# Optimization experiments

Hardware: AMD Instinct MI355X
Metric: run time of the kernel (lower is better)

Reference implementation:

```python
import jax, jax.numpy as jnp
import numpy as np

N_NODES, N_EDGES, B, K = 10000, 100000, 8192, 10
MEM = EMB = TE = EF = 172
HID = 80
MSG = 2 * MEM + TE + EF  # 688


def setup_inputs() -> dict:
    key = jax.random.key(0)
    ks = jax.random.split(key, 24)
    f = jax.random.normal
    inp = {
        'timestamps': jax.random.uniform(ks[0], (B,)) * 100.0,
        'edge_features': f(ks[1], (N_EDGES, EF)),
        'temporal_node_features': f(ks[2], (N_NODES, MEM)),
        'node_mem': 0.1 * f(ks[3], (N_NODES, MEM)),
        'last_updated': jax.random.uniform(ks[4], (N_NODES,)) * 50.0,
        'nbr_edge_times': jax.random.uniform(ks[5], (B, K)) * 100.0,
        # TimeEncode params (fixed init from source)
        'time_w': jnp.asarray(1.0 / 10 ** np.linspace(0, 9, TE), jnp.float32),
        'time_b': jnp.zeros((TE,), jnp.float32),
        # RNNCell params
        'rnn_Wih': 0.05 * f(ks[6], (MEM, MSG)),
        'rnn_Whh': 0.05 * f(ks[7], (MEM, MEM)),
        'rnn_bih': jnp.zeros((MEM,)),
        'rnn_bhh': jnp.zeros((MEM,)),
        # layer linears (n_layers=1)
        'lin1_w': 0.05 * f(ks[8], (EMB, EMB + TE + EF)),
        'lin1_b': jnp.zeros((EMB,)),
        'lin2_w': 0.05 * f(ks[9], (EMB, MEM + TE + EMB)),
        'lin2_b': jnp.zeros((EMB,)),
        # MLP head
        'mlp_w1': 0.05 * f(ks[10], (HID, EMB)),
        'mlp_b1': jnp.zeros((HID,)),
        'mlp_w2': 0.05 * f(ks[11], (10, HID)),
        'mlp_b2': jnp.zeros((10,)),
        'mlp_w3': 0.05 * f(ks[12], (1, 10)),
        'mlp_b3': jnp.zeros((1,)),
        'sources': jax.random.randint(ks[13], (B,), 0, N_NODES),
        'destinations': jax.random.randint(ks[14], (B,), 0, N_NODES),
        'edge_idxs': jax.random.randint(ks[15], (B,), 0, N_EDGES),
        'neighbors': jax.random.randint(ks[16], (B, K), 0, N_NODES),
        'nbr_edge_idxs': jax.random.randint(ks[17], (B, K), 0, N_EDGES),
    }
    return inp


def _time_enc(dt, w, b):
    # cos(Linear(1->D)(t)) from TimeEncode
    return jnp.cos(dt[..., None] * w + b)


def reference(timestamps, edge_features, temporal_node_features, node_mem,
              last_updated, nbr_edge_times, time_w, time_b,
              rnn_Wih, rnn_Whh, rnn_bih, rnn_bhh,
              lin1_w, lin1_b, lin2_w, lin2_b,
              mlp_w1, mlp_b1, mlp_w2, mlp_b2, mlp_w3, mlp_b3,
              sources, destinations, edge_idxs, neighbors, nbr_edge_idxs):
    # ---- get_message: gather memories + edge features + time-delta encoding
    ef = edge_features[edge_idxs]                         # [B, EF]
    src_mem = node_mem[sources]                           # [B, MEM]
    dst_mem = node_mem[destinations]                      # [B, MEM]
    dt = timestamps - last_updated[sources]               # [B]
    msg = jnp.concatenate([src_mem, dst_mem, ef, _time_enc(dt, time_w, time_b)], axis=1)  # [B, MSG]

    # ---- message aggregation: keep LAST message per unique source node
    n = node_mem.shape[0]
    b = sources.shape[0]
    last_idx = jnp.full((n,), -1, jnp.int32).at[sources].max(jnp.arange(b, dtype=jnp.int32))
    upd = last_idx >= 0                                   # [N] nodes receiving a message
    gi = jnp.clip(last_idx, 0)
    node_msg = msg[gi]                                    # [N, MSG]

    # ---- RNNCell memory update (masked to updated nodes)
    h_new = jnp.tanh(node_msg @ rnn_Wih.T + rnn_bih + node_mem @ rnn_Whh.T + rnn_bhh)
    mem = jnp.where(upd[:, None], h_new, node_mem)        # [N, MEM]

    # ---- compute_embedding, n_layers = 1 (layer-0 feats = mem + temporal feats)
    src_feat = mem[sources] + temporal_node_features[sources]      # [B, MEM]
    nbr_feat = mem[neighbors] + temporal_node_features[neighbors]  # [B, K, MEM]
    edge_t_enc = _time_enc(timestamps[:, None] - nbr_edge_times, time_w, time_b)  # [B, K, TE]
    nbr_ef = edge_features[nbr_edge_idxs]                           # [B, K, EF]
    nf = jnp.concatenate([nbr_feat, edge_t_enc, nbr_ef], axis=2)    # [B, K, MEM+TE+EF]
    h1 = jnp.einsum('bkf,ef->bke', nf, lin1_w) + lin1_b             # linear_1
    nbr_sum = jax.nn.relu(jnp.sum(h1, axis=1))                      # sum-aggregate, [B, EMB]
    src_t_enc = _time_enc(jnp.zeros_like(timestamps), time_w, time_b)  # cos(b), [B, TE]
    emb = jnp.concatenate([nbr_sum, src_feat, src_t_enc], axis=1) @ lin2_w.T + lin2_b  # [B, EMB]

    # ---- MLP head (dropout disabled / eval mode) + sigmoid
    h = jax.nn.relu(emb @ mlp_w1.T + mlp_b1)
    h = jax.nn.relu(h @ mlp_w2.T + mlp_b2)
    return jax.nn.sigmoid((h @ mlp_w3.T + mlp_b3)[:, 0])  # [B]
```

## Files before the change

### kernel.cpp

```cpp
#include <hip/hip_runtime.h>
#include <math.h>

#define N_NODES 10000
#define BB 8192
#define KK 10
#define D 172
#define HIDD 80

typedef _Float16 f16;
typedef f16 f16x8 __attribute__((ext_vector_type(8)));
typedef f16 f16x4 __attribute__((ext_vector_type(4)));
typedef float f32x4 __attribute__((ext_vector_type(4)));


__global__ void scatter_last(const int* __restrict__ sources, int* __restrict__ last_idx) {
    int b = blockIdx.x * blockDim.x + threadIdx.x;
    if (b < BB) atomicMax(&last_idx[sources[b]], b);
}

__global__ void compact_nodes(const int* __restrict__ last_idx, int* __restrict__ nid,
                              int* __restrict__ li_arr, int* __restrict__ cnt) {
    int n = blockIdx.x * blockDim.x + threadIdx.x;
    if (n < N_NODES) {
        int li = last_idx[n];
        if (li >= 0) { int p = atomicAdd(cnt, 1); nid[p] = n; li_arr[p] = li; }
    }
}

__global__ __launch_bounds__(256) void conv_weights(
    const float* __restrict__ Wih, const float* __restrict__ Whh,
    const float* __restrict__ lin1_w, const float* __restrict__ lin2_w,
    const float* __restrict__ w1,
    const float* __restrict__ bih, const float* __restrict__ bhh,
    const float* __restrict__ lin2_b, const float* __restrict__ tb,
    const float* __restrict__ node_mem, const float* __restrict__ tnf,
    f16* __restrict__ Wc, f16* __restrict__ W1, f16* __restrict__ W2,
    f16* __restrict__ Wm1, float* __restrict__ bcomb, float* __restrict__ embc,
    f16* __restrict__ FEAT)
{
    const int which = blockIdx.y;
    const int idx = blockIdx.x * 256 + threadIdx.x;
    if (which == 0) {
        if (idx >= 192 * 704) return;
        int n = idx / 704, k = idx % 704, seg = k / 176, kk = k % 176;
        float v = 0.f;
        if (n < D && kk < D) {
            v = Wih[n * 688 + seg * D + kk];
            if (seg == 0) v += Whh[n * D + kk];
        }
        Wc[idx] = (f16)v;
    } else if (which == 1) {
        if (idx >= 192 * 544) return;
        int n = idx / 544, k = idx % 544, seg = k / 176, kk = k % 176;
        float v = 0.f;
        if (n < D && seg < 3 && kk < D) v = lin1_w[n * 516 + seg * D + kk];
        W1[idx] = (f16)v;
    } else if (which == 2) {
        if (idx >= 192 * 352) return;
        int n = idx / 352, k = idx % 352, seg = k / 176, kk = k % 176;
        float v = 0.f;
        if (n < D && kk < D) v = lin2_w[n * 516 + seg * D + kk];
        W2[idx] = (f16)v;
    } else if (which == 3) {
        if (idx >= 80 * 192) return;
        int n = idx / 192, k = idx % 192;
        Wm1[idx] = (f16)((k < D) ? w1[n * D + k] : 0.f);
    } else if (which == 4) {
        if (idx < D) {
            bcomb[idx] = bih[idx] + bhh[idx];
            float acc = lin2_b[idx];
            for (int j = 0; j < D; ++j) acc += lin2_w[idx * 516 + 344 + j] * __cosf(tb[j]);
            embc[idx] = acc;
        }
    } else {
        if (idx >= N_NODES * 22) return;
        int n = idx / 22, k0 = (idx % 22) * 8;
        f16x8 o;
        #pragma unroll
        for (int j = 0; j < 8; ++j) {
            int kk = k0 + j;
            float v = (kk < D) ? node_mem[(size_t)n * D + kk] + tnf[(size_t)n * D + kk] : 0.f;
            o[j] = (f16)v;
        }
        *(f16x8*)(FEAT + (size_t)n * 176 + k0) = o;
    }
}

#define LDA_R 712

__global__ __launch_bounds__(768) void gemm_rnn_fused(
    const f16* __restrict__ Wc, const float* __restrict__ bcomb,
    const int* __restrict__ nid, const int* __restrict__ li_arr, const int* __restrict__ cnt,
    const int* __restrict__ destinations, const int* __restrict__ edge_idxs,
    const float* __restrict__ timestamps, const float* __restrict__ last_updated,
    const float* __restrict__ node_mem, const float* __restrict__ edge_features,
    const float* __restrict__ tw, const float* __restrict__ tb,
    const float* __restrict__ tnf, f16* __restrict__ FEAT)
{
    const int c = *cnt;
    const int R0 = blockIdx.x * 32;
    if (R0 >= c) return;
    __shared__ f16 As[32 * LDA_R];
    __shared__ int s_n[32], s_dst[32], s_ei[32];
    __shared__ float s_dt[32];
    const int t = threadIdx.x;
    if (t < 32) {
        int i = R0 + t; if (i > c - 1) i = c - 1;
        int n = nid[i], li = li_arr[i];
        s_n[t] = n; s_dst[t] = destinations[li]; s_ei[t] = edge_idxs[li];
        s_dt[t] = timestamps[li] - last_updated[n];
    }
    __syncthreads();
    for (int idx = t; idx < 32 * 88; idx += 768) {
        int row = idx / 88, sub = idx - row * 88;
        int seg = sub / 22, cpos = sub - seg * 22, k0 = cpos * 8;
        f16x8 o;
        if (seg < 3) {
            int n = (seg == 0) ? s_n[row] : (seg == 1) ? s_dst[row] : s_ei[row];
            const float* src = ((seg < 2) ? node_mem : edge_features) + (size_t)n * D + k0;
            float4 lo = *(const float4*)src;
            float4 hi = (cpos < 21) ? *(const float4*)(src + 4) : make_float4(0.f, 0.f, 0.f, 0.f);
            o[0] = (f16)lo.x; o[1] = (f16)lo.y; o[2] = (f16)lo.z; o[3] = (f16)lo.w;
            o[4] = (f16)hi.x; o[5] = (f16)hi.y; o[6] = (f16)hi.z; o[7] = (f16)hi.w;
        } else {
            float dt = s_dt[row];
            #pragma unroll
            for (int j = 0; j < 8; ++j) {
                int kk = k0 + j;
                o[j] = (f16)((kk < D) ? __cosf(dt * tw[kk] + tb[kk]) : 0.f);
            }
        }
        *(f16x8*)(As + row * LDA_R + seg * 176 + k0) = o;
    }
    __syncthreads();
    const int w = t >> 6, l = t & 63;
    const int lane16 = l & 15, koff = (l >> 4) * 8;
    const int C0 = w * 16;
    const f16* Al0 = As + lane16 * LDA_R + koff;
    const f16* Al1 = As + (16 + lane16) * LDA_R + koff;
    const f16* Bp  = Wc + (size_t)(C0 + lane16) * 704 + koff;
    f32x4 acc0 = {}, acc1 = {};
    #pragma unroll 2
    for (int s = 0; s < 22; ++s) {
        f16x8 a0 = *(const f16x8*)(Al0 + s * 32);
        f16x8 a1 = *(const f16x8*)(Al1 + s * 32);
        f16x8 b  = *(const f16x8*)(Bp + s * 32);
        acc0 = __builtin_amdgcn_mfma_f32_16x16x32_f16(a0, b, acc0, 0, 0, 0);
        acc1 = __builtin_amdgcn_mfma_f32_16x16x32_f16(a1, b, acc1, 0, 0, 0);
    }
    const int col = C0 + lane16;
    const int rloc = (l >> 4) * 4;
    const float bc = (col < D) ? bcomb[col] : 0.f;
    if (col < D) {
        #pragma unroll
        for (int rh = 0; rh < 2; ++rh) {
            const f32x4& A = rh ? acc1 : acc0;
            #pragma unroll
            for (int reg = 0; reg < 4; ++reg) {
                int rl = rh * 16 + rloc + reg;
                int r = R0 + rl;
                if (r >= c) continue;
                int n = s_n[rl];
                FEAT[(size_t)n * 176 + col] = (f16)(tanhf(A[reg] + bc) + tnf[(size_t)n * D + col]);
            }
        }
    }
}

#define LDA_1 552

__global__ __launch_bounds__(768) void gemm_lin1_fused(
    const f16* __restrict__ W1, const float* __restrict__ lin1_b,
    const f16* __restrict__ FEAT, const float* __restrict__ edge_features,
    const float* __restrict__ timestamps, const float* __restrict__ nbr_edge_times,
    const int* __restrict__ neighbors, const int* __restrict__ nbr_edge_idxs,
    const int* __restrict__ sources,
    const float* __restrict__ tw, const float* __restrict__ tb,
    f16* __restrict__ CAT2)
{
    __shared__ f16 As[32 * LDA_1];
    __shared__ int s_nbr[320], s_nei[320], s_src[32];
    __shared__ float s_net[320], s_ts[32];
    const int t = threadIdx.x;
    const int R0 = blockIdx.x * 32;
    if (t < 320) {
        s_nbr[t] = neighbors[R0 * KK + t];
        s_nei[t] = nbr_edge_idxs[R0 * KK + t];
        s_net[t] = nbr_edge_times[R0 * KK + t];
    } else if (t < 352) {
        s_ts[t - 320] = timestamps[R0 + t - 320];
    } else if (t < 384) {
        s_src[t - 352] = sources[R0 + t - 352];
    }
    __syncthreads();
    for (int idx = t; idx < 32 * 90 + 32 * 22; idx += 768) {
        if (idx < 32 * 90) {
            int row = idx / 90, c = idx - row * 90;
            if (c < 22) {
                int k0 = c * 8;
                f16x8 v[KK];
                #pragma unroll
                for (int k = 0; k < KK; ++k)
                    v[k] = *(const f16x8*)(FEAT + (size_t)s_nbr[row * KK + k] * 176 + k0);
                float a[8] = {};
                #pragma unroll
                for (int k = 0; k < KK; ++k) {
                    #pragma unroll
                    for (int j = 0; j < 8; ++j) a[j] += (float)v[k][j];
                }
                f16x8 o;
                #pragma unroll
                for (int j = 0; j < 8; ++j) o[j] = (f16)a[j];
                *(f16x8*)(As + row * LDA_1 + k0) = o;
            } else if (c < 44) {
                int k0 = (c - 22) * 8;
                float ts = s_ts[row];
                f16x8 o;
                #pragma unroll
                for (int j = 0; j < 8; ++j) {
                    int kk = k0 + j;
                    float a = 0.f;
                    if (kk < D) {
                        float w = tw[kk], bb = tb[kk];
                        #pragma unroll
                        for (int k = 0; k < KK; ++k) a += __cosf((ts - s_net[row * KK + k]) * w + bb);
                    }
                    o[j] = (f16)a;
                }
                *(f16x8*)(As + row * LDA_1 + 176 + k0) = o;
            } else if (c < 88) {
                int cc = c - 44;
                f16x4 o;
                if (cc == 43) {
                    o[0] = o[1] = o[2] = o[3] = (f16)0.f;
                } else {
                    float4 e[KK];
                    #pragma unroll
                    for (int k = 0; k < KK; ++k)
                        e[k] = *(const float4*)(edge_features + (size_t)s_nei[row * KK + k] * D + cc * 4);
                    float a0 = 0.f, a1 = 0.f, a2 = 0.f, a3 = 0.f;
                    #pragma unroll
                    for (int k = 0; k < KK; ++k) { a0 += e[k].x; a1 += e[k].y; a2 += e[k].z; a3 += e[k].w; }
                    o[0] = (f16)a0; o[1] = (f16)a1; o[2] = (f16)a2; o[3] = (f16)a3;
                }
                *(f16x4*)(As + row * LDA_1 + 352 + cc * 4) = o;
            } else {
                f16x8 z = {};
                *(f16x8*)(As + row * LDA_1 + 528 + (c - 88) * 8) = z;
            }
        } else {
            int j = idx - 32 * 90;
            int row = j / 22, cc = j - row * 22;
            *(f16x8*)(CAT2 + (size_t)(R0 + row) * 352 + 176 + cc * 8) =
                *(const f16x8*)(FEAT + (size_t)s_src[row] * 176 + cc * 8);
        }
    }
    __syncthreads();
    const int w = t >> 6, l = t & 63;
    const int lane16 = l & 15, koff = (l >> 4) * 8;
    const int C0 = w * 16;
    const f16* Al0 = As + lane16 * LDA_1 + koff;
    const f16* Al1 = As + (16 + lane16) * LDA_1 + koff;
    const f16* Bp  = W1 + (size_t)(C0 + lane16) * 544 + koff;
    f32x4 acc0 = {}, acc1 = {};
    #pragma unroll 2
    for (int s = 0; s < 17; ++s) {
        f16x8 a0 = *(const f16x8*)(Al0 + s * 32);
        f16x8 a1 = *(const f16x8*)(Al1 + s * 32);
        f16x8 b  = *(const f16x8*)(Bp + s * 32);
        acc0 = __builtin_amdgcn_mfma_f32_16x16x32_f16(a0, b, acc0, 0, 0, 0);
        acc1 = __builtin_amdgcn_mfma_f32_16x16x32_f16(a1, b, acc1, 0, 0, 0);
    }
    const int col = C0 + lane16;
    const int rloc = (l >> 4) * 4;
    const float bb = (col < D) ? 10.0f * lin1_b[col] : 0.f;
    #pragma unroll
    for (int rh = 0; rh < 2; ++rh) {
        const f32x4& A = rh ? acc1 : acc0;
        #pragma unroll
        for (int reg = 0; reg < 4; ++reg) {
            int r = R0 + rh * 16 + rloc + reg;
            CAT2[(size_t)r * 352 + col] = (col < D) ? (f16)fmaxf(A[reg] + bb, 0.f) : (f16)0.f;
        }
    }
}

#define LDE 200

__global__ __launch_bounds__(768) void gemm_lin2_mlp(
    const f16* __restrict__ CAT2, const f16* __restrict__ W2, const float* __restrict__ embc,
    const f16* __restrict__ Wm1, const float* __restrict__ b1,
    const float* __restrict__ w2, const float* __restrict__ b2,
    const float* __restrict__ w3, const float* __restrict__ b3, float* __restrict__ out)
{
    __shared__ f16 Emb[32 * LDE];
    __shared__ float sH[32][84];
    __shared__ float s_w2[10 * HIDD];
    __shared__ float s_b2[10], s_w3[10], s_b3;
    const int t = threadIdx.x;
    const int R0 = blockIdx.x * 32;
    for (int i = t; i < 10 * HIDD; i += 768) s_w2[i] = w2[i];
    if (t < 10) { s_b2[t] = b2[t]; s_w3[t] = w3[t]; }
    if (t == 10) s_b3 = b3[0];
    const int w = t >> 6, l = t & 63;
    const int lane16 = l & 15, koff = (l >> 4) * 8;
    const int rloc = (l >> 4) * 4;
    {
        const int C0 = w * 16;
        const f16* Ap0 = CAT2 + (size_t)(R0 + lane16) * 352 + koff;
        const f16* Ap1 = CAT2 + (size_t)(R0 + 16 + lane16) * 352 + koff;
        const f16* Bp  = W2 + (size_t)(C0 + lane16) * 352 + koff;
        f32x4 acc0 = {}, acc1 = {};
        #pragma unroll 2
        for (int s = 0; s < 11; ++s) {
            f16x8 a0 = *(const f16x8*)(Ap0 + s * 32);
            f16x8 a1 = *(const f16x8*)(Ap1 + s * 32);
            f16x8 b  = *(const f16x8*)(Bp + s * 32);
            acc0 = __builtin_amdgcn_mfma_f32_16x16x32_f16(a0, b, acc0, 0, 0, 0);
            acc1 = __builtin_amdgcn_mfma_f32_16x16x32_f16(a1, b, acc1, 0, 0, 0);
        }
        const int col = C0 + lane16;
        const float ec = (col < D) ? embc[col] : 0.f;
        #pragma unroll
        for (int rh = 0; rh < 2; ++rh) {
            const f32x4& A = rh ? acc1 : acc0;
            #pragma unroll
            for (int reg = 0; reg < 4; ++reg) {
                int r = rh * 16 + rloc + reg;
                Emb[r * LDE + col] = (col < D) ? (f16)(A[reg] + ec) : (f16)0.f;
            }
        }
    }
    __syncthreads();
    if (w < 10) {
        const int C0 = (w >> 1) * 16;
        const int rh = w & 1;
        const f16* Bp = Wm1 + (size_t)(C0 + lane16) * 192 + koff;
        const f16* Al = Emb + (rh * 16 + lane16) * LDE + koff;
        f32x4 acc = {};
        #pragma unroll
        for (int s = 0; s < 6; ++s) {
            f16x8 a = *(const f16x8*)(Al + s * 32);
            f16x8 b = *(const f16x8*)(Bp + s * 32);
            acc = __builtin_amdgcn_mfma_f32_16x16x32_f16(a, b, acc, 0, 0, 0);
        }
        const int col = C0 + lane16;
        #pragma unroll
        for (int reg = 0; reg < 4; ++reg)
            sH[rh * 16 + rloc + reg][col] = fmaxf(acc[reg] + b1[col], 0.f);
    }
    __syncthreads();
    if (t < 32) {
        float h2[10];
        #pragma unroll
        for (int j = 0; j < 10; ++j) h2[j] = s_b2[j];
        for (int f = 0; f < HIDD; ++f) {
            float hv = sH[t][f];
            #pragma unroll
            for (int j = 0; j < 10; ++j) h2[j] = fmaf(hv, s_w2[j * HIDD + f], h2[j]);
        }
        float logit = s_b3;
        #pragma unroll
        for (int j = 0; j < 10; ++j) logit += fmaxf(h2[j], 0.f) * s_w3[j];
        out[R0 + t] = 1.f / (1.f + expf(-logit));
    }
}


extern "C" void kernel_launch(void* const* d_in, const int* in_sizes, int n_in,
                              void* d_out, int out_size, void* d_ws, size_t ws_size,
                              hipStream_t stream) {
    const float* timestamps     = (const float*)d_in[0];
    const float* edge_features  = (const float*)d_in[1];
    const float* tnf            = (const float*)d_in[2];
    const float* node_mem       = (const float*)d_in[3];
    const float* last_updated   = (const float*)d_in[4];
    const float* nbr_edge_times = (const float*)d_in[5];
    const float* time_w         = (const float*)d_in[6];
    const float* time_b         = (const float*)d_in[7];
    const float* Wih            = (const float*)d_in[8];
    const float* Whh            = (const float*)d_in[9];
    const float* bih            = (const float*)d_in[10];
    const float* bhh            = (const float*)d_in[11];
    const float* lin1_w         = (const float*)d_in[12];
    const float* lin1_b         = (const float*)d_in[13];
    const float* lin2_w         = (const float*)d_in[14];
    const float* lin2_b         = (const float*)d_in[15];
    const float* w1             = (const float*)d_in[16];
    const float* b1             = (const float*)d_in[17];
    const float* w2             = (const float*)d_in[18];
    const float* b2             = (const float*)d_in[19];
    const float* w3             = (const float*)d_in[20];
    const float* b3             = (const float*)d_in[21];
    const int* sources          = (const int*)d_in[22];
    const int* destinations     = (const int*)d_in[23];
    const int* edge_idxs        = (const int*)d_in[24];
    const int* neighbors        = (const int*)d_in[25];
    const int* nbr_edge_idxs    = (const int*)d_in[26];
    float* out = (float*)d_out;

    char* p = (char*)d_ws;
    auto bump = [&p](size_t bytes) { char* r = p; p += (bytes + 255) & ~(size_t)255; return r; };
    int* last_idx = (int*)bump(N_NODES * 4);
    int* nid      = (int*)bump(N_NODES * 4);
    int* li_arr   = (int*)bump(N_NODES * 4);
    int* cnt      = (int*)bump(256);
    f16* Wc16     = (f16*)bump((size_t)192 * 704 * 2);
    f16* W1_16    = (f16*)bump((size_t)192 * 544 * 2);
    f16* W2_16    = (f16*)bump((size_t)192 * 352 * 2);
    f16* Wm1_16   = (f16*)bump((size_t)80 * 192 * 2);
    float* bcomb  = (float*)bump(D * 4);
    float* embc   = (float*)bump(D * 4);
    f16* FEAT16   = (f16*)bump((size_t)N_NODES * 176 * 2);
    f16* CAT2_16  = (f16*)bump((size_t)BB * 352 * 2);

    hipMemsetAsync(last_idx, 0xFF, (size_t)N_NODES * 4, stream);
    hipMemsetAsync(cnt, 0, 4, stream);
    hipLaunchKernelGGL(scatter_last, dim3(BB / 256), dim3(256), 0, stream, sources, last_idx);
    hipLaunchKernelGGL(compact_nodes, dim3((N_NODES + 255) / 256), dim3(256), 0, stream,
                       last_idx, nid, li_arr, cnt);

    hipLaunchKernelGGL(conv_weights, dim3(860, 6), dim3(256), 0, stream,
                       Wih, Whh, lin1_w, lin2_w, w1, bih, bhh, lin2_b, time_b,
                       node_mem, tnf, Wc16, W1_16, W2_16, Wm1_16, bcomb, embc, FEAT16);

    hipLaunchKernelGGL(gemm_rnn_fused, dim3((N_NODES + 31) / 32), dim3(768), 0, stream,
                       Wc16, bcomb, nid, li_arr, cnt, destinations, edge_idxs,
                       timestamps, last_updated, node_mem, edge_features,
                       time_w, time_b, tnf, FEAT16);

    hipLaunchKernelGGL(gemm_lin1_fused, dim3(BB / 32), dim3(768), 0, stream,
                       W1_16, lin1_b, FEAT16, edge_features, timestamps, nbr_edge_times,
                       neighbors, nbr_edge_idxs, sources, time_w, time_b, CAT2_16);

    hipLaunchKernelGGL(gemm_lin2_mlp, dim3(BB / 32), dim3(768), 0, stream,
                       CAT2_16, W2_16, embc, Wm1_16, b1, w2, b2, w3, b3, out);
}
```

Baseline: 103.1 us.

## Fuse lin1 and lin2/MLP kernels, fold memsets into prep kernel, halve RNN tile

Merges the lin1 GEMM kernel with the lin2+MLP head kernel so the intermediate concatenated activations stay in shared memory instead of round-tripping through a global CAT2 buffer. The two memsets are folded into the weight-conversion kernel, which now uses a flat 1D grid with range dispatch and is moved ahead of the scatter. The RNN GEMM tile drops from 32 to 16 rows per block, with only 11 waves doing MFMA work, to spread the small update set over more blocks. The fused kernel uses more shared memory per block, which may lower occupancy.

```diff
diff --git a/kernel.cpp b/kernel.cpp
--- a/kernel.cpp
+++ b/kernel.cpp
@@ -26,6 +26,14 @@
         if (li >= 0) { int p = atomicAdd(cnt, 1); nid[p] = n; li_arr[p] = li; }
     }
 }
+
+#define CR0 135168
+#define CR1 (CR0 + 104448)
+#define CR2 (CR1 + 67584)
+#define CR3 (CR2 + 15360)
+#define CR4 (CR3 + 192)
+#define CR5 (CR4 + 220000)
+#define CR6 (CR5 + 10001)
 
 __global__ __launch_bounds__(256) void conv_weights(
     const float* __restrict__ Wih, const float* __restrict__ Whh,
@@ -36,12 +44,10 @@
     const float* __restrict__ node_mem, const float* __restrict__ tnf,
     f16* __restrict__ Wc, f16* __restrict__ W1, f16* __restrict__ W2,
     f16* __restrict__ Wm1, float* __restrict__ bcomb, float* __restrict__ embc,
-    f16* __restrict__ FEAT)
+    f16* __restrict__ FEAT, int* __restrict__ last_idx, int* __restrict__ cnt)
 {
-    const int which = blockIdx.y;
     const int idx = blockIdx.x * 256 + threadIdx.x;
-    if (which == 0) {
-        if (idx >= 192 * 704) return;
+    if (idx < CR0) {
         int n = idx / 704, k = idx % 704, seg = k / 176, kk = k % 176;
         float v = 0.f;
         if (n < D && kk < D) {
@@ -49,32 +55,33 @@
             if (seg == 0) v += Whh[n * D + kk];
         }
         Wc[idx] = (f16)v;
-    } else if (which == 1) {
-        if (idx >= 192 * 544) return;
-        int n = idx / 544, k = idx % 544, seg = k / 176, kk = k % 176;
+    } else if (idx < CR1) {
+        int i = idx - CR0;
+        int n = i / 544, k = i % 544, seg = k / 176, kk = k % 176;
         float v = 0.f;
         if (n < D && seg < 3 && kk < D) v = lin1_w[n * 516 + seg * D + kk];
-        W1[idx] = (f16)v;
-    } else if (which == 2) {
-        if (idx >= 192 * 352) return;
-        int n = idx / 352, k = idx % 352, seg = k / 176, kk = k % 176;
+        W1[i] = (f16)v;
+    } else if (idx < CR2) {
+        int i = idx - CR1;
+        int n = i / 352, k = i % 352, seg = k / 176, kk = k % 176;
         float v = 0.f;
         if (n < D && kk < D) v = lin2_w[n * 516 + seg * D + kk];
-        W2[idx] = (f16)v;
-    } else if (which == 3) {
-        if (idx >= 80 * 192) return;
-        int n = idx / 192, k = idx % 192;
-        Wm1[idx] = (f16)((k < D) ? w1[n * D + k] : 0.f);
-    } else if (which == 4) {
-        if (idx < D) {
-            bcomb[idx] = bih[idx] + bhh[idx];
-            float acc = lin2_b[idx];
-            for (int j = 0; j < D; ++j) acc += lin2_w[idx * 516 + 344 + j] * __cosf(tb[j]);
-            embc[idx] = acc;
-        }
-    } else {
-        if (idx >= N_NODES * 22) return;
-        int n = idx / 22, k0 = (idx % 22) * 8;
+        W2[i] = (f16)v;
+    } else if (idx < CR3) {
+        int i = idx - CR2;
+        int n = i / 192, k = i % 192;
+        Wm1[i] = (f16)((k < D) ? w1[n * D + k] : 0.f);
+    } else if (idx < CR4) {
+        int i = idx - CR3;
+        if (i < D) {
+            bcomb[i] = bih[i] + bhh[i];
+            float acc = lin2_b[i];
+            for (int j = 0; j < D; ++j) acc += lin2_w[i * 516 + 344 + j] * __cosf(tb[j]);
+            embc[i] = acc;
+        }
+    } else if (idx < CR5) {
+        int i = idx - CR4;
+        int n = i / 22, k0 = (i % 22) * 8;
         f16x8 o;
         #pragma unroll
         for (int j = 0; j < 8; ++j) {
@@ -83,6 +90,10 @@
             o[j] = (f16)v;
         }
         *(f16x8*)(FEAT + (size_t)n * 176 + k0) = o;
+    } else if (idx < CR6) {
+        int i = idx - CR5;
+        if (i < N_NODES) last_idx[i] = -1;
+        else *cnt = 0;
     }
 }
 
@@ -98,20 +109,20 @@
     const float* __restrict__ tnf, f16* __restrict__ FEAT)
 {
     const int c = *cnt;
-    const int R0 = blockIdx.x * 32;
+    const int R0 = blockIdx.x * 16;
     if (R0 >= c) return;
-    __shared__ f16 As[32 * LDA_R];
-    __shared__ int s_n[32], s_dst[32], s_ei[32];
-    __shared__ float s_dt[32];
+    __shared__ f16 As[16 * LDA_R];
+    __shared__ int s_n[16], s_dst[16], s_ei[16];
+    __shared__ float s_dt[16];
     const int t = threadIdx.x;
-    if (t < 32) {
+    if (t < 16) {
         int i = R0 + t; if (i > c - 1) i = c - 1;
         int n = nid[i], li = li_arr[i];
         s_n[t] = n; s_dst[t] = destinations[li]; s_ei[t] = edge_idxs[li];
         s_dt[t] = timestamps[li] - last_updated[n];
     }
     __syncthreads();
-    for (int idx = t; idx < 32 * 88; idx += 768) {
+    for (int idx = t; idx < 16 * 88; idx += 768) {
         int row = idx / 88, sub = idx - row * 88;
         int seg = sub / 22, cpos = sub - seg * 22, k0 = cpos * 8;
         f16x8 o;
@@ -134,63 +145,73 @@
     }
     __syncthreads();
     const int w = t >> 6, l = t & 63;
+    if (w >= 11) return;
     const int lane16 = l & 15, koff = (l >> 4) * 8;
     const int C0 = w * 16;
-    const f16* Al0 = As + lane16 * LDA_R + koff;
-    const f16* Al1 = As + (16 + lane16) * LDA_R + koff;
-    const f16* Bp  = Wc + (size_t)(C0 + lane16) * 704 + koff;
-    f32x4 acc0 = {}, acc1 = {};
+    const f16* Al = As + lane16 * LDA_R + koff;
+    const f16* Bp = Wc + (size_t)(C0 + lane16) * 704 + koff;
+    f32x4 acc = {};
     #pragma unroll 2
     for (int s = 0; s < 22; ++s) {
-        f16x8 a0 = *(const f16x8*)(Al0 + s * 32);
-        f16x8 a1 = *(const f16x8*)(Al1 + s * 32);
-        f16x8 b  = *(const f16x8*)(Bp + s * 32);
-        acc0 = __builtin_amdgcn_mfma_f32_16x16x32_f16(a0, b, acc0, 0, 0, 0);
-        acc1 = __builtin_amdgcn_mfma_f32_16x16x32_f16(a1, b, acc1, 0, 0, 0);
+        f16x8 a = *(const f16x8*)(Al + s * 32);
+        f16x8 b = *(const f16x8*)(Bp + s * 32);
+        acc = __builtin_amdgcn_mfma_f32_16x16x32_f16(a, b, acc, 0, 0, 0);
     }
     const int col = C0 + lane16;
     const int rloc = (l >> 4) * 4;
-    const float bc = (col < D) ? bcomb[col] : 0.f;
     if (col < D) {
-        #pragma unroll
-        for (int rh = 0; rh < 2; ++rh) {
-            const f32x4& A = rh ? acc1 : acc0;
-            #pragma unroll
-            for (int reg = 0; reg < 4; ++reg) {
-                int rl = rh * 16 + rloc + reg;
-                int r = R0 + rl;
-                if (r >= c) continue;
-                int n = s_n[rl];
-                FEAT[(size_t)n * 176 + col] = (f16)(tanhf(A[reg] + bc) + tnf[(size_t)n * D + col]);
-            }
+        const float bc = bcomb[col];
+        #pragma unroll
+        for (int reg = 0; reg < 4; ++reg) {
+            int rl = rloc + reg;
+            int r = R0 + rl;
+            if (r >= c) continue;
+            int n = s_n[rl];
+            FEAT[(size_t)n * 176 + col] = (f16)(tanhf(acc[reg] + bc) + tnf[(size_t)n * D + col]);
         }
     }
 }
 
 #define LDA_1 552
-
-__global__ __launch_bounds__(768) void gemm_lin1_fused(
+#define LDA_2 360
+#define LDE  200
+
+__global__ __launch_bounds__(768) void embed_fused(
     const f16* __restrict__ W1, const float* __restrict__ lin1_b,
+    const f16* __restrict__ W2, const float* __restrict__ embc,
+    const f16* __restrict__ Wm1, const float* __restrict__ b1,
+    const float* __restrict__ w2, const float* __restrict__ b2,
+    const float* __restrict__ w3, const float* __restrict__ b3,
     const f16* __restrict__ FEAT, const float* __restrict__ edge_features,
     const float* __restrict__ timestamps, const float* __restrict__ nbr_edge_times,
     const int* __restrict__ neighbors, const int* __restrict__ nbr_edge_idxs,
     const int* __restrict__ sources,
     const float* __restrict__ tw, const float* __restrict__ tb,
-    f16* __restrict__ CAT2)
+    float* __restrict__ out)
 {
     __shared__ f16 As[32 * LDA_1];
+    __shared__ f16 Acat[32 * LDA_2];
+    __shared__ float sH[32][84];
+    __shared__ float s_w2[10 * HIDD];
+    __shared__ float s_b2[10], s_w3[10], s_b3;
     __shared__ int s_nbr[320], s_nei[320], s_src[32];
     __shared__ float s_net[320], s_ts[32];
     const int t = threadIdx.x;
     const int R0 = blockIdx.x * 32;
-    if (t < 320) {
-        s_nbr[t] = neighbors[R0 * KK + t];
-        s_nei[t] = nbr_edge_idxs[R0 * KK + t];
-        s_net[t] = nbr_edge_times[R0 * KK + t];
-    } else if (t < 352) {
-        s_ts[t - 320] = timestamps[R0 + t - 320];
-    } else if (t < 384) {
-        s_src[t - 352] = sources[R0 + t - 352];
+    for (int i = t; i < 10 * HIDD; i += 768) s_w2[i] = w2[i];
+    if (t < 10) { s_b2[t] = b2[t]; s_w3[t] = w3[t]; }
+    if (t == 10) s_b3 = b3[0];
+    if (t >= 64 && t < 384) {
+        int u = t - 64;
+        s_nbr[u] = neighbors[R0 * KK + u];
+    } else if (t >= 384 && t < 704) {
+        int u = t - 384;
+        s_nei[u] = nbr_edge_idxs[R0 * KK + u];
+        s_net[u] = nbr_edge_times[R0 * KK + u];
+    } else if (t >= 704 && t < 736) {
+        s_ts[t - 704] = timestamps[R0 + t - 704];
+    } else if (t >= 736) {
+        s_src[t - 736] = sources[R0 + t - 736];
     }
     __syncthreads();
     for (int idx = t; idx < 32 * 90 + 32 * 22; idx += 768) {
@@ -251,70 +272,53 @@
         } else {
             int j = idx - 32 * 90;
             int row = j / 22, cc = j - row * 22;
-            *(f16x8*)(CAT2 + (size_t)(R0 + row) * 352 + 176 + cc * 8) =
+            *(f16x8*)(Acat + row * LDA_2 + 176 + cc * 8) =
                 *(const f16x8*)(FEAT + (size_t)s_src[row] * 176 + cc * 8);
         }
     }
     __syncthreads();
-    const int w = t >> 6, l = t & 63;
-    const int lane16 = l & 15, koff = (l >> 4) * 8;
-    const int C0 = w * 16;
-    const f16* Al0 = As + lane16 * LDA_1 + koff;
-    const f16* Al1 = As + (16 + lane16) * LDA_1 + koff;
-    const f16* Bp  = W1 + (size_t)(C0 + lane16) * 544 + koff;
-    f32x4 acc0 = {}, acc1 = {};
-    #pragma unroll 2
-    for (int s = 0; s < 17; ++s) {
-        f16x8 a0 = *(const f16x8*)(Al0 + s * 32);
-        f16x8 a1 = *(const f16x8*)(Al1 + s * 32);
-        f16x8 b  = *(const f16x8*)(Bp + s * 32);
-        acc0 = __builtin_amdgcn_mfma_f32_16x16x32_f16(a0, b, acc0, 0, 0, 0);
-        acc1 = __builtin_amdgcn_mfma_f32_16x16x32_f16(a1, b, acc1, 0, 0, 0);
-    }
-    const int col = C0 + lane16;
-    const int rloc = (l >> 4) * 4;
-    const float bb = (col < D) ? 10.0f * lin1_b[col] : 0.f;
-    #pragma unroll
-    for (int rh = 0; rh < 2; ++rh) {
-        const f32x4& A = rh ? acc1 : acc0;
-        #pragma unroll
-        for (int reg = 0; reg < 4; ++reg) {
-            int r = R0 + rh * 16 + rloc + reg;
-            CAT2[(size_t)r * 352 + col] = (col < D) ? (f16)fmaxf(A[reg] + bb, 0.f) : (f16)0.f;
-        }
-    }
-}
-
-#define LDE 200
-
-__global__ __launch_bounds__(768) void gemm_lin2_mlp(
-    const f16* __restrict__ CAT2, const f16* __restrict__ W2, const float* __restrict__ embc,
-    const f16* __restrict__ Wm1, const float* __restrict__ b1,
-    const float* __restrict__ w2, const float* __restrict__ b2,
-    const float* __restrict__ w3, const float* __restrict__ b3, float* __restrict__ out)
-{
-    __shared__ f16 Emb[32 * LDE];
-    __shared__ float sH[32][84];
-    __shared__ float s_w2[10 * HIDD];
-    __shared__ float s_b2[10], s_w3[10], s_b3;
-    const int t = threadIdx.x;
-    const int R0 = blockIdx.x * 32;
-    for (int i = t; i < 10 * HIDD; i += 768) s_w2[i] = w2[i];
-    if (t < 10) { s_b2[t] = b2[t]; s_w3[t] = w3[t]; }
-    if (t == 10) s_b3 = b3[0];
     const int w = t >> 6, l = t & 63;
     const int lane16 = l & 15, koff = (l >> 4) * 8;
     const int rloc = (l >> 4) * 4;
+    const int C0 = w * 16;
     {
-        const int C0 = w * 16;
-        const f16* Ap0 = CAT2 + (size_t)(R0 + lane16) * 352 + koff;
-        const f16* Ap1 = CAT2 + (size_t)(R0 + 16 + lane16) * 352 + koff;
+        const f16* Al0 = As + lane16 * LDA_1 + koff;
+        const f16* Al1 = As + (16 + lane16) * LDA_1 + koff;
+        const f16* Bp  = W1 + (size_t)(C0 + lane16) * 544 + koff;
+        f32x4 acc0 = {}, acc1 = {};
+        #pragma unroll 2
+        for (int s = 0; s < 17; ++s) {
+            f16x8 a0 = *(const f16x8*)(Al0 + s * 32);
+            f16x8 a1 = *(const f16x8*)(Al1 + s * 32);
+            f16x8 b  = *(const f16x8*)(Bp + s * 32);
+            acc0 = __builtin_amdgcn_mfma_f32_16x16x32_f16(a0, b, acc0, 0, 0, 0);
+            acc1 = __builtin_amdgcn_mfma_f32_16x16x32_f16(a1, b, acc1, 0, 0, 0);
+        }
+        const int col = C0 + lane16;
+        if (col < 176) {
+            const float bb = (col < D) ? 10.0f * lin1_b[col] : 0.f;
+            #pragma unroll
+            for (int rh = 0; rh < 2; ++rh) {
+                const f32x4& A = rh ? acc1 : acc0;
+                #pragma unroll
+                for (int reg = 0; reg < 4; ++reg) {
+                    int r = rh * 16 + rloc + reg;
+                    Acat[r * LDA_2 + col] = (col < D) ? (f16)fmaxf(A[reg] + bb, 0.f) : (f16)0.f;
+                }
+            }
+        }
+    }
+    __syncthreads();
+    f16* Emb = As;
+    {
+        const f16* Al0 = Acat + lane16 * LDA_2 + koff;
+        const f16* Al1 = Acat + (16 + lane16) * LDA_2 + koff;
         const f16* Bp  = W2 + (size_t)(C0 + lane16) * 352 + koff;
         f32x4 acc0 = {}, acc1 = {};
         #pragma unroll 2
         for (int s = 0; s < 11; ++s) {
-            f16x8 a0 = *(const f16x8*)(Ap0 + s * 32);
-            f16x8 a1 = *(const f16x8*)(Ap1 + s * 32);
+            f16x8 a0 = *(const f16x8*)(Al0 + s * 32);
+            f16x8 a1 = *(const f16x8*)(Al1 + s * 32);
             f16x8 b  = *(const f16x8*)(Bp + s * 32);
             acc0 = __builtin_amdgcn_mfma_f32_16x16x32_f16(a0, b, acc0, 0, 0, 0);
             acc1 = __builtin_amdgcn_mfma_f32_16x16x32_f16(a1, b, acc1, 0, 0, 0);
@@ -333,9 +337,9 @@
     }
     __syncthreads();
     if (w < 10) {
-        const int C0 = (w >> 1) * 16;
+        const int Cm = (w >> 1) * 16;
         const int rh = w & 1;
-        const f16* Bp = Wm1 + (size_t)(C0 + lane16) * 192 + koff;
+        const f16* Bp = Wm1 + (size_t)(Cm + lane16) * 192 + koff;
         const f16* Al = Emb + (rh * 16 + lane16) * LDE + koff;
         f32x4 acc = {};
         #pragma unroll
@@ -344,7 +348,7 @@
             f16x8 b = *(const f16x8*)(Bp + s * 32);
             acc = __builtin_amdgcn_mfma_f32_16x16x32_f16(a, b, acc, 0, 0, 0);
         }
-        const int col = C0 + lane16;
+        const int col = Cm + lane16;
         #pragma unroll
         for (int reg = 0; reg < 4; ++reg)
             sH[rh * 16 + rloc + reg][col] = fmaxf(acc[reg] + b1[col], 0.f);
@@ -412,27 +416,23 @@
     float* bcomb  = (float*)bump(D * 4);
     float* embc   = (float*)bump(D * 4);
     f16* FEAT16   = (f16*)bump((size_t)N_NODES * 176 * 2);
-    f16* CAT2_16  = (f16*)bump((size_t)BB * 352 * 2);
-
-    hipMemsetAsync(last_idx, 0xFF, (size_t)N_NODES * 4, stream);
-    hipMemsetAsync(cnt, 0, 4, stream);
+
+    hipLaunchKernelGGL(conv_weights, dim3((CR6 + 255) / 256), dim3(256), 0, stream,
+                       Wih, Whh, lin1_w, lin2_w, w1, bih, bhh, lin2_b, time_b,
+                       node_mem, tnf, Wc16, W1_16, W2_16, Wm1_16, bcomb, embc,
+                       FEAT16, last_idx, cnt);
+
     hipLaunchKernelGGL(scatter_last, dim3(BB / 256), dim3(256), 0, stream, sources, last_idx);
     hipLaunchKernelGGL(compact_nodes, dim3((N_NODES + 255) / 256), dim3(256), 0, stream,
                        last_idx, nid, li_arr, cnt);
 
-    hipLaunchKernelGGL(conv_weights, dim3(860, 6), dim3(256), 0, stream,
-                       Wih, Whh, lin1_w, lin2_w, w1, bih, bhh, lin2_b, time_b,
-                       node_mem, tnf, Wc16, W1_16, W2_16, Wm1_16, bcomb, embc, FEAT16);
-
-    hipLaunchKernelGGL(gemm_rnn_fused, dim3((N_NODES + 31) / 32), dim3(768), 0, stream,
+    hipLaunchKernelGGL(gemm_rnn_fused, dim3((N_NODES + 15) / 16), dim3(768), 0, stream,
                        Wc16, bcomb, nid, li_arr, cnt, destinations, edge_idxs,
                        timestamps, last_updated, node_mem, edge_features,
                        time_w, time_b, tnf, FEAT16);
 
-    hipLaunchKernelGGL(gemm_lin1_fused, dim3(BB / 32), dim3(768), 0, stream,
-                       W1_16, lin1_b, FEAT16, edge_features, timestamps, nbr_edge_times,
-                       neighbors, nbr_edge_idxs, sources, time_w, time_b, CAT2_16);
-
-    hipLaunchKernelGGL(gemm_lin2_mlp, dim3(BB / 32), dim3(768), 0, stream,
-                       CAT2_16, W2_16, embc, Wm1_16, b1, w2, b2, w3, b3, out);
-}
+    hipLaunchKernelGGL(embed_fused, dim3(BB / 32), dim3(768), 0, stream,
+                       W1_16, lin1_b, W2_16, embc, Wm1_16, b1, w2, b2, w3, b3,
+                       FEAT16, edge_features, timestamps, nbr_edge_times,
+                       neighbors, nbr_edge_idxs, sources, time_w, time_b, out);
+}
```

Result: faster. 90.62 us (-12.1%).
